# Kernel optimization log

Hardware: AMD Instinct MI355X
Metric: run time of the kernel (lower is better)

Reference implementation:

```python
import jax, jax.numpy as jnp
import numpy as np

MAX_LENGTH = 252
HID = 768
MLP = 770
NLAB = 36


def setup_inputs() -> dict:
    key = jax.random.key(0)
    ks = jax.random.split(key, 7)
    B = 2
    hidden = jax.random.normal(ks[0], (B, MAX_LENGTH + 1, HID), dtype=jnp.float32)
    pred_spans = jnp.sort(jax.random.randint(ks[1], (B, 2), 0, MAX_LENGTH), axis=1)
    span_mask = jax.random.randint(ks[2], (MAX_LENGTH, MAX_LENGTH), 0, 2).astype(jnp.int32)
    W1 = jax.random.normal(ks[3], (MLP, 2 * HID + 1), dtype=jnp.float32) * 0.02
    b1 = jax.random.normal(ks[4], (MLP,), dtype=jnp.float32) * 0.02
    W2 = jax.random.normal(ks[5], (NLAB, MLP), dtype=jnp.float32) * 0.02
    b2 = jax.random.normal(ks[6], (NLAB,), dtype=jnp.float32) * 0.02
    return {"hidden": hidden, "pred_spans": pred_spans, "span_mask": span_mask,
            "W1": W1, "b1": b1, "W2": W2, "b2": b2}


def reference(hidden, pred_spans, span_mask, W1, b1, W2, b2):
    L = MAX_LENGTH
    B = hidden.shape[0]
    vecs = hidden[:, 1:L + 1, :]                      # [B, L, 768] (skip [CLS])
    # Split concat-weight: feat = [vec_i, vec_j, indicator]
    W1i = W1[:, :HID]                                 # [770, 768]
    W1j = W1[:, HID:2 * HID]                          # [770, 768]
    w1c = W1[:, 2 * HID]                              # [770]
    Ai = jnp.einsum('bld,hd->blh', vecs, W1i)         # [B, L, 770]
    Aj = jnp.einsum('bld,hd->blh', vecs, W1j)         # [B, L, 770]
    # Predicate-span indicator: 2 if (i,j)==pred_span; 1 if strictly inside
    # combinations_with_replacement(start..end) minus (start,end); else 0.
    ii = jnp.arange(L)[:, None]
    jj = jnp.arange(L)[None, :]
    s = pred_spans[:, 0][:, None, None]
    e = pred_spans[:, 1][:, None, None]
    eq = (ii == s) & (jj == e)
    inside = (s <= ii) & (ii <= jj) & (jj <= e)
    ind = jnp.where(eq, 2.0, jnp.where(inside, 1.0, 0.0)).astype(hidden.dtype)  # [B,L,L]
    h = Ai[:, :, None, :] + Aj[:, None, :, :] + ind[..., None] * w1c + b1       # [B,L,L,770]
    h = jax.nn.relu(h)
    out = jnp.einsum('bijh,kh->bijk', h, W2) + b2     # [B, L, L, 36]
    valid = (span_mask >= 1)[None, :, :, None]
    out = jnp.where(valid, out, 0.0)                  # invalid pairs -> exact zeros
    out = out.reshape(B, L * L, NLAB)                 # pair dim = 63504
    res = jax.nn.log_softmax(out, axis=1)             # softmax over span pairs
    return jnp.transpose(res, (0, 2, 1))              # [B, 36, L*L]
```

## Files before the change

kernel.cpp:

```cpp
#include <hip/hip_runtime.h>
#include <hip/hip_fp16.h>
#include <math.h>

#define L 252
#define HID 768
#define MLP 770
#define NLAB 36
#define NB 2
#define M1 (NB*L)
#define N1 (2*MLP)
#define LL (L*L)
#define LL4 (LL/4)
#define KC 25
#define KC1 24
#define NT1P 100
#define NMT 32

typedef float f32x4 __attribute__((ext_vector_type(4)));
typedef _Float16 half8 __attribute__((ext_vector_type(8)));
typedef _Float16 half2v __attribute__((ext_vector_type(2)));

#define AJF_OFF 0
#define AJF_FLOATS 204800
#define AIB_OFF (AJF_OFF + AJF_FLOATS)
#define AIB_FLOATS 604800
#define W2F_OFF (AIB_OFF + AIB_FLOATS)
#define W2F_FLOATS 19200
#define PART_OFF (W2F_OFF + W2F_FLOATS)
#define PART_FLOATS (72*1024*2)
#define W1F_OFF (PART_OFF + PART_FLOATS)
#define W1F_FLOATS (KC1*NT1P*64*4)
#define VBF_OFF (W1F_OFF + W1F_FLOATS)
#define VBF_FLOATS (NMT*KC1*64*4)
#define NW1F (KC1*NT1P*64)
#define NW2F (KC*3*64)
#define NVBF (NMT*KC1*64)

__device__ __forceinline__ void dma16(const void* g, void* l) {
  __builtin_amdgcn_global_load_lds(
      (const __attribute__((address_space(1))) unsigned int*)g,
      (__attribute__((address_space(3))) unsigned int*)l, 16, 0, 0);
}

__device__ __forceinline__ unsigned short f16b(float x) {
  _Float16 h = (_Float16)x;
  return *reinterpret_cast<unsigned short*>(&h);
}

#define WAIT_VM0() __builtin_amdgcn_s_waitcnt(0x0F70)
#define WAIT_VM3() __builtin_amdgcn_s_waitcnt(0x0F73)
#define WAIT_VM5() __builtin_amdgcn_s_waitcnt(0x0F75)

__global__ __launch_bounds__(256) void pack_kernel(const float* __restrict__ W1,
                                                   const float* __restrict__ W2,
                                                   const float* __restrict__ hid,
                                                   float* __restrict__ ws) {
  const int total = NW1F + NW2F + NVBF;
  int idx = blockIdx.x * 256 + threadIdx.x;
  if (idx >= total) return;
  if (idx < NW1F) {
    int kc = idx / (NT1P * 64);
    int rem = idx - kc * (NT1P * 64);
    int nt = rem / 64, lane = rem - nt * 64;
    int n = nt * 16 + (lane & 15);
    int kb = kc * 32 + (lane >> 4) * 8;
    unsigned int u[4];
#pragma unroll
    for (int p = 0; p < 4; p++) {
      unsigned short us[2];
#pragma unroll
      for (int q = 0; q < 2; q++) {
        int k = kb + 2 * p + q;
        float v = 0.f;
        if (n < N1) v = (n < MLP) ? W1[(size_t)n * 1537 + k]
                                  : W1[(size_t)(n - MLP) * 1537 + HID + k];
        us[q] = f16b(v);
      }
      u[p] = (unsigned int)us[0] | ((unsigned int)us[1] << 16);
    }
    ((uint4*)(ws + W1F_OFF))[idx] = make_uint4(u[0], u[1], u[2], u[3]);
  } else if (idx < NW1F + NW2F) {
    int e2 = idx - NW1F;
    int kc = e2 / 192, rem = e2 - kc * 192;
    int tile = rem / 64, lane = rem - tile * 64;
    int label = tile * 16 + (lane & 15);
    int kb = kc * 32 + (lane >> 4) * 8;
    unsigned int u[4];
#pragma unroll
    for (int p = 0; p < 4; p++) {
      unsigned short us[2];
#pragma unroll
      for (int q = 0; q < 2; q++) {
        int k = kb + 2 * p + q;
        float v = (label < NLAB && k < MLP) ? W2[label * MLP + k] : 0.f;
        us[q] = f16b(v);
      }
      u[p] = (unsigned int)us[0] | ((unsigned int)us[1] << 16);
    }
    ((uint4*)(ws + W2F_OFF))[e2] = make_uint4(u[0], u[1], u[2], u[3]);
  } else {
    int e3 = idx - NW1F - NW2F;
    int mt = e3 / (KC1 * 64);
    int rem = e3 - mt * (KC1 * 64);
    int kc = rem / 64, lane = rem - kc * 64;
    int m = mt * 16 + (lane & 15);
    int kb = kc * 32 + (lane >> 4) * 8;
    unsigned int u[4] = {0u, 0u, 0u, 0u};
    if (m < M1) {
      int b = (m >= L) ? 1 : 0;
      const float* src = hid + ((size_t)(b * (L + 1) + 1 + (m - b * L))) * HID + kb;
      float4 v0 = *(const float4*)src;
      float4 v1 = *(const float4*)(src + 4);
      float vv[8] = {v0.x, v0.y, v0.z, v0.w, v1.x, v1.y, v1.z, v1.w};
#pragma unroll
      for (int p = 0; p < 4; p++)
        u[p] = (unsigned int)f16b(vv[2 * p]) | ((unsigned int)f16b(vv[2 * p + 1]) << 16);
    }
    ((uint4*)(ws + VBF_OFF))[e3] = make_uint4(u[0], u[1], u[2], u[3]);
  }
}

__global__ __launch_bounds__(256, 2) void gemm1_kernel(const float* __restrict__ b1,
                                                       const float* __restrict__ W1,
                                                       const float* __restrict__ ws_ro,
                                                       unsigned short* __restrict__ AJF,
                                                       unsigned short* __restrict__ AiBh) {
  __shared__ char sm[36864];
  int t = threadIdx.x;
  int wave = t >> 6, lane = t & 63, lj = lane & 15, kh = lane >> 4;
  int nt0 = blockIdx.x * 2;
  int mt = blockIdx.y * 4 + wave;
  int m0 = mt * 16;
  const uint4* vbf = (const uint4*)(ws_ro + VBF_OFF) + (size_t)mt * KC1 * 64 + lane;
  const uint4* w1f = (const uint4*)(ws_ro + W1F_OFF);
  char* WB = sm + wave * 9216;
  char* bA = WB;
  char* bB = WB + 3072;
  char* bC = WB + 6144;

  f32x4 acc[2];
#pragma unroll
  for (int nt = 0; nt < 2; nt++) acc[nt] = (f32x4)(0.f);
  union FU { unsigned u[4]; half8 h8; };

  dma16(vbf, bA);
#pragma unroll
  for (int q = 0; q < 2; q++)
    dma16(&w1f[(size_t)(0 * NT1P + nt0 + q) * 64 + lane], bA + 1024 + q * 1024);
  dma16(vbf + 64, bB);
#pragma unroll
  for (int q = 0; q < 2; q++)
    dma16(&w1f[(size_t)(1 * NT1P + nt0 + q) * 64 + lane], bB + 1024 + q * 1024);

  for (int kc = 0; kc < KC1; kc++) {
    WAIT_VM3();
    uint4 av = *(const uint4*)(bA + lane * 16);
    uint4 bv[2];
#pragma unroll
    for (int q = 0; q < 2; q++) bv[q] = *(const uint4*)(bA + 1024 + q * 1024 + lane * 16);
    __builtin_amdgcn_sched_barrier(0);
    int kn = kc + 2; if (kn > KC1 - 1) kn = KC1 - 1;
    dma16(vbf + kn * 64, bC);
#pragma unroll
    for (int q = 0; q < 2; q++)
      dma16(&w1f[(size_t)(kn * NT1P + nt0 + q) * 64 + lane], bC + 1024 + q * 1024);
    __builtin_amdgcn_sched_barrier(0);
    { char* tmp = bA; bA = bB; bB = bC; bC = tmp; }
    FU af; af.u[0] = av.x; af.u[1] = av.y; af.u[2] = av.z; af.u[3] = av.w;
#pragma unroll
    for (int q = 0; q < 2; q++) {
      FU bf; bf.u[0] = bv[q].x; bf.u[1] = bv[q].y; bf.u[2] = bv[q].z; bf.u[3] = bv[q].w;
      acc[q] = __builtin_amdgcn_mfma_f32_16x16x32_f16(af.h8, bf.h8, acc[q], 0, 0, 0);
    }
  }

#pragma unroll
  for (int nt = 0; nt < 2; nt++) {
    int nn = (nt0 + nt) * 16 + lj;
    if (nn >= N1) continue;
    if (nn < MLP) {
      float b1v = b1[nn];
      float wv = W1[(size_t)nn * 1537 + 1536];
#pragma unroll
      for (int r = 0; r < 4; r++) {
        int mm = m0 + kh * 4 + r;
        if (mm < M1) {
          float a = acc[nt][r] + b1v;
          AiBh[(size_t)(0 * M1 + mm) * 800 + nn] = f16b(a);
          AiBh[(size_t)(1 * M1 + mm) * 800 + nn] = f16b(a + wv);
          AiBh[(size_t)(2 * M1 + mm) * 800 + nn] = f16b(a + 2.f * wv);
        }
      }
    } else {
      int hh = nn - MLP;
      int kcq = hh >> 5, kk = hh & 31;
      int l2hi = (kk >> 3) << 4, ee = kk & 7;
#pragma unroll
      for (int r = 0; r < 4; r++) {
        int mm = m0 + kh * 4 + r;
        if (mm < M1) {
          int bb2 = (mm >= L) ? 1 : 0;
          int jg = mm - bb2 * L;
          size_t rec = ((size_t)((bb2 * KC + kcq) * 16 + (jg >> 4)) * 64 + (l2hi | (jg & 15)));
          AJF[rec * 8 + ee] = f16b(acc[nt][r]);
        }
      }
    }
  }
}

__global__ __launch_bounds__(256, 2) void main_kernel(
    const unsigned short* __restrict__ AJF,
    const unsigned short* __restrict__ AiBh,
    const uint4* __restrict__ wfr,
    const float* __restrict__ b2,
    const int* __restrict__ spans,
    const int* __restrict__ smask,
    float* __restrict__ out,
    float* __restrict__ part) {
  __shared__ char sm[61440];
  int t = threadIdx.x;
  int wave = t >> 6, lane = t & 63, lj = lane & 15, kh = lane >> 4;
  int j0 = blockIdx.x * 64;
  int i0 = blockIdx.y * 4;
  int b = blockIdx.z;
  int s = spans[2 * b], e = spans[2 * b + 1];
  int j = j0 + wave * 16 + lj;

  int poff[4];
#pragma unroll
  for (int ii = 0; ii < 4; ii++) {
    int i = i0 + ii;
    int ind = 0;
    if (i == s && j == e) ind = 2;
    else if (s <= i && i <= j && j <= e) ind = 1;
    poff[ii] = 1024 + ((ind * 4 + ii) * 4 + kh) * 16;
  }

  const unsigned short* aj_g = AJF + ((size_t)((b * KC + 0) * 16 + (j0 >> 4) + wave) * 64 + lane) * 8;
  int pr = lane >> 2; if (pr > 11) pr = 11;
  int pt = pr >> 2, pii = pr & 3, pc = lane & 3;
  const unsigned short* p_g = AiBh + (size_t)(pt * M1 + b * L + i0 + pii) * 800 + pc * 8;
  const uint4* wf_g = wfr + lane;
  char* WB = sm + wave * 15360;
  char* bA = WB;
  char* bB = WB + 5120;
  char* bC = WB + 10240;

  f32x4 acc[4][3];
#pragma unroll
  for (int ii = 0; ii < 4; ii++)
#pragma unroll
    for (int tl = 0; tl < 3; tl++) acc[ii][tl] = (f32x4)(0.f);
  union FU { unsigned u[4]; half8 h8; };
  union U2 { unsigned u; half2v h; };

  dma16(aj_g, bA);
  dma16(p_g, bA + 1024);
  dma16(&wf_g[0 * 64], bA + 2048);
  dma16(&wf_g[1 * 64], bA + 3072);
  dma16(&wf_g[2 * 64], bA + 4096);
  dma16(aj_g + 8192, bB);
  dma16(p_g + 32, bB + 1024);
  dma16(&wf_g[3 * 64], bB + 2048);
  dma16(&wf_g[4 * 64], bB + 3072);
  dma16(&wf_g[5 * 64], bB + 4096);

  for (int kc = 0; kc < KC; kc++) {
    WAIT_VM5();
    uint4 av = *(const uint4*)(bA + lane * 16);
    uint4 w0 = *(const uint4*)(bA + 2048 + lane * 16);
    uint4 w1 = *(const uint4*)(bA + 3072 + lane * 16);
    uint4 w2v = *(const uint4*)(bA + 4096 + lane * 16);
    uint4 pv[4];
#pragma unroll
    for (int ii = 0; ii < 4; ii++) pv[ii] = *(const uint4*)(bA + poff[ii]);
    __builtin_amdgcn_sched_barrier(0);
    int kn = kc + 2; if (kn > KC - 1) kn = KC - 1;
    dma16(aj_g + (size_t)kn * 8192, bC);
    dma16(p_g + kn * 32, bC + 1024);
    dma16(&wf_g[(kn * 3 + 0) * 64], bC + 2048);
    dma16(&wf_g[(kn * 3 + 1) * 64], bC + 3072);
    dma16(&wf_g[(kn * 3 + 2) * 64], bC + 4096);
    __builtin_amdgcn_sched_barrier(0);
    { char* tmp = bA; bA = bB; bB = bC; bC = tmp; }
    unsigned avu[4] = {av.x, av.y, av.z, av.w};
    FU wf0, wf1, wf2;
    wf0.u[0] = w0.x; wf0.u[1] = w0.y; wf0.u[2] = w0.z; wf0.u[3] = w0.w;
    wf1.u[0] = w1.x; wf1.u[1] = w1.y; wf1.u[2] = w1.z; wf1.u[3] = w1.w;
    wf2.u[0] = w2v.x; wf2.u[1] = w2v.y; wf2.u[2] = w2v.z; wf2.u[3] = w2v.w;
#pragma unroll
    for (int ii = 0; ii < 4; ii++) {
      unsigned pu[4] = {pv[ii].x, pv[ii].y, pv[ii].z, pv[ii].w};
      FU fr;
#pragma unroll
      for (int q = 0; q < 4; q++) {
        U2 a, p, r;
        a.u = avu[q]; p.u = pu[q];
        half2v sum = a.h + p.h;
        half2v zz = (half2v)((_Float16)0);
        r.h = __builtin_elementwise_max(sum, zz);
        fr.u[q] = r.u;
      }
      acc[ii][0] = __builtin_amdgcn_mfma_f32_16x16x32_f16(fr.h8, wf0.h8, acc[ii][0], 0, 0, 0);
      acc[ii][1] = __builtin_amdgcn_mfma_f32_16x16x32_f16(fr.h8, wf1.h8, acc[ii][1], 0, 0, 0);
      acc[ii][2] = __builtin_amdgcn_mfma_f32_16x16x32_f16(fr.h8, wf2.h8, acc[ii][2], 0, 0, 0);
    }
  }

  float v[4][3][4];
#pragma unroll
  for (int ii = 0; ii < 4; ii++) {
    int i = i0 + ii;
    int smv[4];
#pragma unroll
    for (int r = 0; r < 4; r++) {
      int jr = j0 + wave * 16 + kh * 4 + r;
      smv[r] = (jr < L) ? smask[(size_t)i * L + jr] : 0;
    }
#pragma unroll
    for (int tl = 0; tl < 3; tl++) {
      int label = tl * 16 + lj;
      bool lab_ok = label < NLAB;
      float bbv = lab_ok ? b2[label] : 0.f;
#pragma unroll
      for (int r = 0; r < 4; r++) {
        int jr = j0 + wave * 16 + kh * 4 + r;
        float vv = -1e30f;
        if (jr < L && lab_ok) {
          vv = (smv[r] >= 1) ? acc[ii][tl][r] + bbv : 0.f;
          out[(size_t)(b * NLAB + label) * LL + (size_t)i * L + jr] = vv;
        }
        v[ii][tl][r] = vv;
      }
    }
  }
#pragma unroll
  for (int tl = 0; tl < 3; tl++) {
    float mx = -1e30f;
#pragma unroll
    for (int ii = 0; ii < 4; ii++)
#pragma unroll
      for (int r = 0; r < 4; r++) mx = fmaxf(mx, v[ii][tl][r]);
    mx = fmaxf(mx, __shfl_xor(mx, 16, 64));
    mx = fmaxf(mx, __shfl_xor(mx, 32, 64));
    float ssum = 0.f;
#pragma unroll
    for (int ii = 0; ii < 4; ii++)
#pragma unroll
      for (int r = 0; r < 4; r++) {
        float vv = v[ii][tl][r];
        ssum += (vv > -1e29f) ? __expf(vv - mx) : 0.f;
      }
    ssum += __shfl_xor(ssum, 16, 64);
    ssum += __shfl_xor(ssum, 32, 64);
    int label = tl * 16 + lj;
    if (kh == 0 && label < NLAB) {
      int slot = (blockIdx.x * 63 + blockIdx.y) * 4 + wave;
      float2* pp = (float2*)part + (size_t)(b * NLAB + label) * 1024 + slot;
      *pp = make_float2(mx, ssum);
    }
  }
}

__global__ __launch_bounds__(256) void finish_kernel(const float* __restrict__ part,
                                                     float* __restrict__ out) {
  int bk = blockIdx.y, cx = blockIdx.x;
  int t = threadIdx.x, wave = t >> 6, lane = t & 63;
  const float2* pp = (const float2*)part + (size_t)bk * 1024;
  float m = -1e30f, ss = 0.f;
  for (int idx = t; idx < 1008; idx += 256) {
    float2 q = pp[idx];
    if (q.x > m) { ss = ss * __expf(m - q.x) + q.y; m = q.x; }
    else ss += q.y * __expf(q.x - m);
  }
#pragma unroll
  for (int o = 1; o < 64; o <<= 1) {
    float m2 = __shfl_xor(m, o, 64);
    float s2 = __shfl_xor(ss, o, 64);
    if (m2 > m) { ss = ss * __expf(m - m2) + s2; m = m2; }
    else ss += s2 * __expf(m2 - m);
  }
  __shared__ float rm[4], rs[4], lsh;
  if (lane == 0) { rm[wave] = m; rs[wave] = ss; }
  __syncthreads();
  if (t == 0) {
    float M = rm[0], S = rs[0];
#pragma unroll
    for (int w = 1; w < 4; w++) {
      float m2 = rm[w], s2 = rs[w];
      if (m2 > M) { S = S * __expf(M - m2) + s2; M = m2; }
      else S += s2 * __expf(m2 - M);
    }
    lsh = M + logf(S);
  }
  __syncthreads();
  float l = lsh;
  float4* po = (float4*)(out + (size_t)bk * LL);
  int start = cx * 1985;
  int end = start + 1985; if (end > LL4) end = LL4;
  for (int idx = start + t; idx < end; idx += 256) {
    float4 v = po[idx];
    v.x -= l; v.y -= l; v.z -= l; v.w -= l;
    po[idx] = v;
  }
}

extern "C" void kernel_launch(void* const* d_in, const int* in_sizes, int n_in,
                              void* d_out, int out_size, void* d_ws, size_t ws_size,
                              hipStream_t stream) {
  const float* hidden = (const float*)d_in[0];
  const int* spans    = (const int*)d_in[1];
  const int* smask    = (const int*)d_in[2];
  const float* W1     = (const float*)d_in[3];
  const float* b1     = (const float*)d_in[4];
  const float* W2     = (const float*)d_in[5];
  const float* b2     = (const float*)d_in[6];
  float* ws = (float*)d_ws;
  unsigned short* AJF  = (unsigned short*)(ws + AJF_OFF);
  unsigned short* AiBh = (unsigned short*)(ws + AIB_OFF);
  const uint4* wfr     = (const uint4*)(ws + W2F_OFF);
  float* part          = ws + PART_OFF;
  float* out = (float*)d_out;

  const int total_pack = NW1F + NW2F + NVBF;
  pack_kernel<<<(total_pack + 255) / 256, 256, 0, stream>>>(W1, W2, hidden, ws);
  gemm1_kernel<<<dim3(50, 8), 256, 0, stream>>>(b1, W1, ws, AJF, AiBh);
  main_kernel<<<dim3(4, 63, NB), 256, 0, stream>>>(AJF, AiBh, wfr, b2, spans, smask, out, part);
  finish_kernel<<<dim3(8, NB * NLAB), 256, 0, stream>>>(part, out);
}
```

Before: 130.4 us.

## Fuse weight/activation packing into gemm1 and drop separate pack kernel

Removes the standalone pack kernel. Each gemm1 block now converts its own 32-column W1 slice to fp16 MFMA fragments directly in shared memory, and converts hidden rows to fp16 in registers from global memory with one-step prefetch. W2 fragment packing is spread across the y=0 blocks. This saves one launch and the workspace round trip. In exchange, W1 conversion is repeated across the 8 row-blocks, and the async LDS DMA pipeline is replaced by plain register prefetch.

```diff
diff --git a/kernel.cpp b/kernel.cpp
--- a/kernel.cpp
+++ b/kernel.cpp
@@ -28,13 +28,7 @@
 #define W2F_FLOATS 19200
 #define PART_OFF (W2F_OFF + W2F_FLOATS)
 #define PART_FLOATS (72*1024*2)
-#define W1F_OFF (PART_OFF + PART_FLOATS)
-#define W1F_FLOATS (KC1*NT1P*64*4)
-#define VBF_OFF (W1F_OFF + W1F_FLOATS)
-#define VBF_FLOATS (NMT*KC1*64*4)
-#define NW1F (KC1*NT1P*64)
 #define NW2F (KC*3*64)
-#define NVBF (NMT*KC1*64)
 
 __device__ __forceinline__ void dma16(const void* g, void* l) {
   __builtin_amdgcn_global_load_lds(
@@ -47,23 +41,48 @@
   return *reinterpret_cast<unsigned short*>(&h);
 }
 
-#define WAIT_VM0() __builtin_amdgcn_s_waitcnt(0x0F70)
-#define WAIT_VM3() __builtin_amdgcn_s_waitcnt(0x0F73)
 #define WAIT_VM5() __builtin_amdgcn_s_waitcnt(0x0F75)
 
-__global__ __launch_bounds__(256) void pack_kernel(const float* __restrict__ W1,
-                                                   const float* __restrict__ W2,
-                                                   const float* __restrict__ hid,
-                                                   float* __restrict__ ws) {
-  const int total = NW1F + NW2F + NVBF;
-  int idx = blockIdx.x * 256 + threadIdx.x;
-  if (idx >= total) return;
-  if (idx < NW1F) {
-    int kc = idx / (NT1P * 64);
-    int rem = idx - kc * (NT1P * 64);
-    int nt = rem / 64, lane = rem - nt * 64;
-    int n = nt * 16 + (lane & 15);
-    int kb = kc * 32 + (lane >> 4) * 8;
+__global__ __launch_bounds__(256, 3) void gemm1_kernel(
+    const float* __restrict__ b1, const float* __restrict__ W1,
+    const float* __restrict__ W2, const float* __restrict__ hidden,
+    float* __restrict__ ws, unsigned short* __restrict__ AJF,
+    unsigned short* __restrict__ AiBh) {
+  __shared__ char sm[49152];
+  int t = threadIdx.x;
+  int wave = t >> 6, lane = t & 63, lj = lane & 15, kh = lane >> 4;
+  int nt0 = blockIdx.x * 2;
+  int mt = blockIdx.y * 4 + wave;
+  int m0 = mt * 16;
+  union FU { unsigned u[4]; half8 h8; };
+
+  if (blockIdx.y == 0 && t < 96) {
+    int e2 = blockIdx.x * 96 + t;
+    int kc = e2 / 192, rem = e2 - kc * 192;
+    int tile = rem / 64, ln = rem - tile * 64;
+    int label = tile * 16 + (ln & 15);
+    int kb = kc * 32 + (ln >> 4) * 8;
+    unsigned int u[4];
+#pragma unroll
+    for (int p = 0; p < 4; p++) {
+      unsigned short us[2];
+#pragma unroll
+      for (int q = 0; q < 2; q++) {
+        int k = kb + 2 * p + q;
+        float v = (label < NLAB && k < MLP) ? W2[label * MLP + k] : 0.f;
+        us[q] = f16b(v);
+      }
+      u[p] = (unsigned int)us[0] | ((unsigned int)us[1] << 16);
+    }
+    ((uint4*)(ws + W2F_OFF))[e2] = make_uint4(u[0], u[1], u[2], u[3]);
+  }
+
+#pragma unroll
+  for (int r = 0; r < 12; r++) {
+    int e = t + 256 * r;
+    int le = e & 63, ntt = (e >> 6) & 1, kcc = e >> 7;
+    int n = (nt0 + ntt) * 16 + (le & 15);
+    int kb = kcc * 32 + (le >> 4) * 8;
     unsigned int u[4];
 #pragma unroll
     for (int p = 0; p < 4; p++) {
@@ -78,100 +97,42 @@
       }
       u[p] = (unsigned int)us[0] | ((unsigned int)us[1] << 16);
     }
-    ((uint4*)(ws + W1F_OFF))[idx] = make_uint4(u[0], u[1], u[2], u[3]);
-  } else if (idx < NW1F + NW2F) {
-    int e2 = idx - NW1F;
-    int kc = e2 / 192, rem = e2 - kc * 192;
-    int tile = rem / 64, lane = rem - tile * 64;
-    int label = tile * 16 + (lane & 15);
-    int kb = kc * 32 + (lane >> 4) * 8;
-    unsigned int u[4];
+    *(uint4*)(sm + (size_t)e * 16) = make_uint4(u[0], u[1], u[2], u[3]);
+  }
+  __syncthreads();
+
+  int mrow = m0 + lj;
+  const bool mvalid = mrow < M1;
+  if (mrow >= M1) mrow = M1 - 1;
+  int bb = (mrow >= L) ? 1 : 0;
+  const float* aptr = hidden + ((size_t)(bb * (L + 1) + 1 + (mrow - bb * L))) * HID + kh * 8;
+
+  f32x4 acc[2];
+  acc[0] = (f32x4)(0.f);
+  acc[1] = (f32x4)(0.f);
+  float4 pa0 = *(const float4*)(aptr);
+  float4 pa1 = *(const float4*)(aptr + 4);
+
+  for (int kc = 0; kc < KC1; kc++) {
+    float4 c0 = pa0, c1 = pa1;
+    int kn = (kc < KC1 - 1) ? kc + 1 : kc;
+    pa0 = *(const float4*)(aptr + kn * 32);
+    pa1 = *(const float4*)(aptr + kn * 32 + 4);
+    uint4 bv0 = *(const uint4*)(sm + (size_t)(kc * 2 + 0) * 1024 + lane * 16);
+    uint4 bv1 = *(const uint4*)(sm + (size_t)(kc * 2 + 1) * 1024 + lane * 16);
+    float cf[8] = {c0.x, c0.y, c0.z, c0.w, c1.x, c1.y, c1.z, c1.w};
+    FU af;
 #pragma unroll
     for (int p = 0; p < 4; p++) {
-      unsigned short us[2];
-#pragma unroll
-      for (int q = 0; q < 2; q++) {
-        int k = kb + 2 * p + q;
-        float v = (label < NLAB && k < MLP) ? W2[label * MLP + k] : 0.f;
-        us[q] = f16b(v);
-      }
-      u[p] = (unsigned int)us[0] | ((unsigned int)us[1] << 16);
-    }
-    ((uint4*)(ws + W2F_OFF))[e2] = make_uint4(u[0], u[1], u[2], u[3]);
-  } else {
-    int e3 = idx - NW1F - NW2F;
-    int mt = e3 / (KC1 * 64);
-    int rem = e3 - mt * (KC1 * 64);
-    int kc = rem / 64, lane = rem - kc * 64;
-    int m = mt * 16 + (lane & 15);
-    int kb = kc * 32 + (lane >> 4) * 8;
-    unsigned int u[4] = {0u, 0u, 0u, 0u};
-    if (m < M1) {
-      int b = (m >= L) ? 1 : 0;
-      const float* src = hid + ((size_t)(b * (L + 1) + 1 + (m - b * L))) * HID + kb;
-      float4 v0 = *(const float4*)src;
-      float4 v1 = *(const float4*)(src + 4);
-      float vv[8] = {v0.x, v0.y, v0.z, v0.w, v1.x, v1.y, v1.z, v1.w};
-#pragma unroll
-      for (int p = 0; p < 4; p++)
-        u[p] = (unsigned int)f16b(vv[2 * p]) | ((unsigned int)f16b(vv[2 * p + 1]) << 16);
-    }
-    ((uint4*)(ws + VBF_OFF))[e3] = make_uint4(u[0], u[1], u[2], u[3]);
-  }
-}
-
-__global__ __launch_bounds__(256, 2) void gemm1_kernel(const float* __restrict__ b1,
-                                                       const float* __restrict__ W1,
-                                                       const float* __restrict__ ws_ro,
-                                                       unsigned short* __restrict__ AJF,
-                                                       unsigned short* __restrict__ AiBh) {
-  __shared__ char sm[36864];
-  int t = threadIdx.x;
-  int wave = t >> 6, lane = t & 63, lj = lane & 15, kh = lane >> 4;
-  int nt0 = blockIdx.x * 2;
-  int mt = blockIdx.y * 4 + wave;
-  int m0 = mt * 16;
-  const uint4* vbf = (const uint4*)(ws_ro + VBF_OFF) + (size_t)mt * KC1 * 64 + lane;
-  const uint4* w1f = (const uint4*)(ws_ro + W1F_OFF);
-  char* WB = sm + wave * 9216;
-  char* bA = WB;
-  char* bB = WB + 3072;
-  char* bC = WB + 6144;
-
-  f32x4 acc[2];
-#pragma unroll
-  for (int nt = 0; nt < 2; nt++) acc[nt] = (f32x4)(0.f);
-  union FU { unsigned u[4]; half8 h8; };
-
-  dma16(vbf, bA);
-#pragma unroll
-  for (int q = 0; q < 2; q++)
-    dma16(&w1f[(size_t)(0 * NT1P + nt0 + q) * 64 + lane], bA + 1024 + q * 1024);
-  dma16(vbf + 64, bB);
-#pragma unroll
-  for (int q = 0; q < 2; q++)
-    dma16(&w1f[(size_t)(1 * NT1P + nt0 + q) * 64 + lane], bB + 1024 + q * 1024);
-
-  for (int kc = 0; kc < KC1; kc++) {
-    WAIT_VM3();
-    uint4 av = *(const uint4*)(bA + lane * 16);
-    uint4 bv[2];
-#pragma unroll
-    for (int q = 0; q < 2; q++) bv[q] = *(const uint4*)(bA + 1024 + q * 1024 + lane * 16);
-    __builtin_amdgcn_sched_barrier(0);
-    int kn = kc + 2; if (kn > KC1 - 1) kn = KC1 - 1;
-    dma16(vbf + kn * 64, bC);
-#pragma unroll
-    for (int q = 0; q < 2; q++)
-      dma16(&w1f[(size_t)(kn * NT1P + nt0 + q) * 64 + lane], bC + 1024 + q * 1024);
-    __builtin_amdgcn_sched_barrier(0);
-    { char* tmp = bA; bA = bB; bB = bC; bC = tmp; }
-    FU af; af.u[0] = av.x; af.u[1] = av.y; af.u[2] = av.z; af.u[3] = av.w;
-#pragma unroll
-    for (int q = 0; q < 2; q++) {
-      FU bf; bf.u[0] = bv[q].x; bf.u[1] = bv[q].y; bf.u[2] = bv[q].z; bf.u[3] = bv[q].w;
-      acc[q] = __builtin_amdgcn_mfma_f32_16x16x32_f16(af.h8, bf.h8, acc[q], 0, 0, 0);
-    }
+      float f0 = mvalid ? cf[2 * p] : 0.f;
+      float f1 = mvalid ? cf[2 * p + 1] : 0.f;
+      af.u[p] = (unsigned int)f16b(f0) | ((unsigned int)f16b(f1) << 16);
+    }
+    FU bf0, bf1;
+    bf0.u[0] = bv0.x; bf0.u[1] = bv0.y; bf0.u[2] = bv0.z; bf0.u[3] = bv0.w;
+    bf1.u[0] = bv1.x; bf1.u[1] = bv1.y; bf1.u[2] = bv1.z; bf1.u[3] = bv1.w;
+    acc[0] = __builtin_amdgcn_mfma_f32_16x16x32_f16(af.h8, bf0.h8, acc[0], 0, 0, 0);
+    acc[1] = __builtin_amdgcn_mfma_f32_16x16x32_f16(af.h8, bf1.h8, acc[1], 0, 0, 0);
   }
 
 #pragma unroll
@@ -423,9 +384,7 @@
   float* part          = ws + PART_OFF;
   float* out = (float*)d_out;
 
-  const int total_pack = NW1F + NW2F + NVBF;
-  pack_kernel<<<(total_pack + 255) / 256, 256, 0, stream>>>(W1, W2, hidden, ws);
-  gemm1_kernel<<<dim3(50, 8), 256, 0, stream>>>(b1, W1, ws, AJF, AiBh);
+  gemm1_kernel<<<dim3(50, 8), 256, 0, stream>>>(b1, W1, W2, hidden, ws, AJF, AiBh);
   main_kernel<<<dim3(4, 63, NB), 256, 0, stream>>>(AJF, AiBh, wfr, b2, spans, smask, out, part);
   finish_kernel<<<dim3(8, NB * NLAB), 256, 0, stream>>>(part, out);
 }
```

Result: slower. 152.2 us (+16.7%).
